# Kernel optimization log

Hardware: AMD Instinct MI355X
Metric: run time of the kernel (lower is better)

The kernel has to match this reference:

```python
import jax, jax.numpy as jnp
import numpy as np

L, H, D, A, T = 2, 8, 512, 64, 256  # layers, heads, model_dim, attention_dim, target_dim
B, S = 2, 2048
EPS = 1e-5


def _ln(x, g, b):
    m = jnp.mean(x, axis=-1, keepdims=True)
    v = jnp.mean((x - m) ** 2, axis=-1, keepdims=True)
    return (x - m) / jnp.sqrt(v + EPS) * g + b


def setup_inputs() -> dict:
    key = jax.random.key(0)
    ks = jax.random.split(key, 16)
    s = 0.02
    inp = {
        "x": jax.random.normal(ks[0], (B, S, D), jnp.float32),
        # per-head QKV projections, stacked over layers and heads
        "Wq": jax.random.normal(ks[1], (L, H, D, A), jnp.float32) * s,
        "bq": jnp.zeros((L, H, A), jnp.float32),
        "Wk": jax.random.normal(ks[2], (L, H, D, A), jnp.float32) * s,
        "bk": jnp.zeros((L, H, A), jnp.float32),
        "Wv": jax.random.normal(ks[3], (L, H, D, A), jnp.float32) * s,
        "bv": jnp.zeros((L, H, A), jnp.float32),
        # output projection of concatenated heads: [H*A, D]
        "Wo": jax.random.normal(ks[4], (L, H * A, D), jnp.float32) * s,
        "bo": jnp.zeros((L, D), jnp.float32),
        # AddNorm after attention
        "ln1_g": jnp.ones((L, D), jnp.float32),
        "ln1_b": jnp.zeros((L, D), jnp.float32),
        # FFN (hidden_dim == model_dim in this module)
        "W1": jax.random.normal(ks[5], (L, D, D), jnp.float32) * s,
        "b1": jnp.zeros((L, D), jnp.float32),
        "W2": jax.random.normal(ks[6], (L, D, D), jnp.float32) * s,
        "b2": jnp.zeros((L, D), jnp.float32),
        # AddNorm after FFN
        "ln2_g": jnp.ones((L, D), jnp.float32),
        "ln2_b": jnp.zeros((L, D), jnp.float32),
        # final projection to target_dim
        "Wp": jax.random.normal(ks[7], (D, T), jnp.float32) * s,
        "bp": jnp.zeros((T,), jnp.float32),
    }
    return inp


def reference(x, Wq, bq, Wk, bk, Wv, bv, Wo, bo, ln1_g, ln1_b,
              W1, b1, W2, b2, ln2_g, ln2_b, Wp, bp):
    scale = 1.0 / jnp.sqrt(jnp.asarray(A, x.dtype))
    for i in range(L):
        # batched per-head QKV projections (math identical to per-head Linears)
        q = jnp.einsum('bsd,hda->bhsa', x, Wq[i]) + bq[i][:, None, :]
        k = jnp.einsum('bsd,hda->bhsa', x, Wk[i]) + bk[i][:, None, :]
        v = jnp.einsum('bsd,hda->bhsa', x, Wv[i]) + bv[i][:, None, :]
        scores = jnp.einsum('bhsa,bhta->bhst', q, k) * scale  # [B,H,S,S]
        attn = jax.nn.softmax(scores, axis=-1)
        heads = jnp.einsum('bhst,bhta->bhsa', attn, v)        # [B,H,S,A]
        concat = heads.transpose(0, 2, 1, 3).reshape(x.shape[0], x.shape[1], H * A)
        mha = concat @ Wo[i] + bo[i]
        x = _ln(x + mha, ln1_g[i], ln1_b[i])
        ffn = jax.nn.relu(x @ W1[i] + b1[i]) @ W2[i] + b2[i]
        x = _ln(x + ffn, ln2_g[i], ln2_b[i])
    return x @ Wp + bp
```

## Files before the change

### kernel.cpp

```cpp
#include <hip/hip_runtime.h>
#include <hip/hip_bf16.h>

#define MDIM 4096
#define DDIM 512
#define ADIM 64
#define HHEADS 8
#define SLEN 2048
#define TDIM 256
#define SPLIT 4

typedef __attribute__((ext_vector_type(8))) short short8;
typedef __attribute__((ext_vector_type(16))) float f32x16;

__device__ __forceinline__ unsigned short f2bf(float f) {
    union { __hip_bfloat16 h; unsigned short u; } c;
    c.h = __float2bfloat16(f);
    return c.u;
}
__device__ __forceinline__ float bf2f(short s) {
    return __uint_as_float((unsigned)(unsigned short)s << 16);
}

#define N1 524288
#define N2 524288
#define NP 131072
__global__ __launch_bounds__(256) void prep_k(
    const float* __restrict__ Wq, const float* __restrict__ Wk, const float* __restrict__ Wv,
    const float* __restrict__ Wo, const float* __restrict__ W1, const float* __restrict__ W2,
    const float* __restrict__ Wp, const float* __restrict__ x,
    short* __restrict__ Wqt, short* __restrict__ Wkt, short* __restrict__ Wvt,
    short* __restrict__ Wot, short* __restrict__ W1t, short* __restrict__ W2t,
    short* __restrict__ Wpt, short* __restrict__ xbf)
{
    long idx = (long)blockIdx.x * 256 + threadIdx.x;
    if (idx < 3L * N1) {
        int t = (int)(idx / N1);
        int r = (int)(idx % N1);
        int a = r & 63, k = (r >> 6) & 511, hh = r >> 15;
        const float* src = (t == 0) ? Wq : (t == 1) ? Wk : Wv;
        short* dst = (t == 0) ? Wqt : (t == 1) ? Wkt : Wvt;
        dst[((size_t)hh << 15) + (a << 9) + k] = (short)f2bf(src[r]);
        return;
    }
    idx -= 3L * N1;
    if (idx < 3L * N2) {
        int t = (int)(idx / N2);
        int r = (int)(idx % N2);
        int n = r & 511, k = (r >> 9) & 511, i = r >> 18;
        const float* src = (t == 0) ? Wo : (t == 1) ? W1 : W2;
        short* dst = (t == 0) ? Wot : (t == 1) ? W1t : W2t;
        dst[((size_t)i << 18) + (n << 9) + k] = (short)f2bf(src[r]);
        return;
    }
    idx -= 3L * N2;
    if (idx < NP) {
        int r = (int)idx;
        int n = r & 255, k = r >> 8;
        Wpt[n * 512 + k] = (short)f2bf(Wp[r]);
        return;
    }
    idx -= NP;
    xbf[idx] = (short)f2bf(x[idx]);
}

#define LDT 66
__global__ __launch_bounds__(256, 2) void gemm_bf(
    const short* __restrict__ A, const short* __restrict__ Bt,
    const float* __restrict__ bias, void* __restrict__ Cout,
    int M, int N, int K, int flags)
{
    __shared__ short As[64 * LDT];
    __shared__ short Bs[64 * LDT];
    const int tid = threadIdx.x;
    const int wave = tid >> 6, lane = tid & 63;
    const int l31 = lane & 31, hi = lane >> 5;
    const int wm = wave >> 1, wn = wave & 1;
    const int m0 = blockIdx.y * 64, n0 = blockIdx.x * 64;

    f32x16 acc;
#pragma unroll
    for (int r = 0; r < 16; ++r) acc[r] = 0.f;

    const int sr = tid >> 2;
    const int sc = (tid & 3) * 16;

    for (int k0 = 0; k0 < K; k0 += 64) {
        __syncthreads();
        *(short8*)&As[sr * LDT + sc]     = *(const short8*)&A[(size_t)(m0 + sr) * K + k0 + sc];
        *(short8*)&As[sr * LDT + sc + 8] = *(const short8*)&A[(size_t)(m0 + sr) * K + k0 + sc + 8];
        *(short8*)&Bs[sr * LDT + sc]     = *(const short8*)&Bt[(size_t)(n0 + sr) * K + k0 + sc];
        *(short8*)&Bs[sr * LDT + sc + 8] = *(const short8*)&Bt[(size_t)(n0 + sr) * K + k0 + sc + 8];
        __syncthreads();

        short8 af[4], bfm[4];
#pragma unroll
        for (int ks = 0; ks < 4; ++ks) {
            af[ks]  = *(const short8*)&As[(wm * 32 + l31) * LDT + ks * 16 + hi * 8];
            bfm[ks] = *(const short8*)&Bs[(wn * 32 + l31) * LDT + ks * 16 + hi * 8];
        }
#pragma unroll
        for (int ks = 0; ks < 4; ++ks)
            acc = __builtin_amdgcn_mfma_f32_32x32x16_bf16(af[ks], bfm[ks], acc, 0, 0, 0);
    }

    const int col = n0 + wn * 32 + l31;
    const float bb = bias[col];
    const int rbase = m0 + wm * 32 + 4 * hi;
#pragma unroll
    for (int r = 0; r < 16; ++r) {
        int row = rbase + (r & 3) + 8 * (r >> 2);
        float v = acc[r] + bb;
        if (flags & 1) v = fmaxf(v, 0.f);
        if (flags & 2) ((short*)Cout)[(size_t)row * N + col] = (short)f2bf(v);
        else           ((float*)Cout)[(size_t)row * N + col] = v;
    }
}

#define EXPC 0.1803368801111244f

__global__ __launch_bounds__(256, 2) void qkv_bf(
    const short* __restrict__ A,
    const short* __restrict__ Wqt, const short* __restrict__ Wkt, const short* __restrict__ Wvt,
    const float* __restrict__ bq, const float* __restrict__ bk, const float* __restrict__ bv,
    short* __restrict__ Oq, short* __restrict__ Ok, short* __restrict__ Ov)
{
    __shared__ short As[128 * LDT];
    __shared__ short Bs[64 * LDT];
    const int tid = threadIdx.x;
    const int wave = tid >> 6, lane = tid & 63;
    const int l31 = lane & 31, hi = lane >> 5;
    const int wm = wave >> 1, wn = wave & 1;
    const int m0 = blockIdx.y * 128;
    const int nt = blockIdx.x;
    const int which = nt >> 3, h = nt & 7;

    const short* Bt = ((which == 0) ? Wqt : (which == 1) ? Wkt : Wvt) + (size_t)h * 64 * 512;
    const float* bias = ((which == 0) ? bq : (which == 1) ? bk : bv) + h * 64;
    short* Out = (which == 0) ? Oq : (which == 1) ? Ok : Ov;

    f32x16 acc[2];
#pragma unroll
    for (int ms = 0; ms < 2; ++ms)
#pragma unroll
        for (int r = 0; r < 16; ++r) acc[ms][r] = 0.f;

    const int sr = tid >> 3;
    const int sc = (tid & 7) * 8;

    for (int k0 = 0; k0 < 512; k0 += 64) {
        __syncthreads();
#pragma unroll
        for (int p = 0; p < 4; ++p)
            *(short8*)&As[(p * 32 + sr) * LDT + sc] =
                *(const short8*)&A[(size_t)(m0 + p * 32 + sr) * 512 + k0 + sc];
#pragma unroll
        for (int p = 0; p < 2; ++p)
            *(short8*)&Bs[(p * 32 + sr) * LDT + sc] =
                *(const short8*)&Bt[(size_t)(p * 32 + sr) * 512 + k0 + sc];
        __syncthreads();

        short8 af[2][4], bfm[4];
#pragma unroll
        for (int ms = 0; ms < 2; ++ms)
#pragma unroll
            for (int ks = 0; ks < 4; ++ks)
                af[ms][ks] = *(const short8*)&As[(wm * 64 + ms * 32 + l31) * LDT + ks * 16 + hi * 8];
#pragma unroll
        for (int ks = 0; ks < 4; ++ks)
            bfm[ks] = *(const short8*)&Bs[(wn * 32 + l31) * LDT + ks * 16 + hi * 8];
#pragma unroll
        for (int ms = 0; ms < 2; ++ms)
#pragma unroll
            for (int ks = 0; ks < 4; ++ks)
                acc[ms] = __builtin_amdgcn_mfma_f32_32x32x16_bf16(af[ms][ks], bfm[ks], acc[ms], 0, 0, 0);
    }

    const int a = wn * 32 + l31;
    const float bb = bias[a];
    const int b = m0 >> 11;
    const int sb = (m0 & (SLEN - 1)) + wm * 64;
    const int bh = b * HHEADS + h;

    if (which == 0) {
        short* Ob = Out + (size_t)bh * SLEN * 64;
#pragma unroll
        for (int ms = 0; ms < 2; ++ms)
#pragma unroll
            for (int r = 0; r < 16; ++r) {
                int s = sb + ms * 32 + (r & 3) + 8 * (r >> 2) + 4 * hi;
                Ob[(size_t)s * 64 + a] = (short)f2bf((acc[ms][r] + bb) * EXPC);
            }
    } else if (which == 1) {
        short* Ob = Out + (size_t)bh * SLEN * 64;
#pragma unroll
        for (int ms = 0; ms < 2; ++ms)
#pragma unroll
            for (int r = 0; r < 16; ++r) {
                int s = sb + ms * 32 + (r & 3) + 8 * (r >> 2) + 4 * hi;
                Ob[(size_t)s * 64 + a] = (short)f2bf(acc[ms][r] + bb);
            }
    } else {
        short* Ob = Out + ((size_t)bh * 64 + a) * SLEN;
#pragma unroll
        for (int ms = 0; ms < 2; ++ms)
#pragma unroll
            for (int g = 0; g < 4; ++g) {
                int s = sb + ms * 32 + 8 * g + 4 * hi;
                ushort4 w;
                w.x = f2bf(acc[ms][4 * g + 0] + bb);
                w.y = f2bf(acc[ms][4 * g + 1] + bb);
                w.z = f2bf(acc[ms][4 * g + 2] + bb);
                w.w = f2bf(acc[ms][4 * g + 3] + bb);
                *(ushort4*)&Ob[s] = w;
            }
    }
}

__global__ __launch_bounds__(256, 2) void attn_mfma(
    const short* __restrict__ Qb, const short* __restrict__ Kb,
    const short* __restrict__ Vtb, short* __restrict__ Op,
    float* __restrict__ lp)
{
    __shared__ short Ks[64 * 72];
    __shared__ short Vs[64 * 72];

    const int tid = threadIdx.x;
    const int wid = tid >> 6;
    const int lane = tid & 63;
    const int l31 = lane & 31;
    const int hi = lane >> 5;

    const int qt = blockIdx.x;
    const int bh = blockIdx.y;
    const int sp = blockIdx.z;

    const short* Qg = Qb + (size_t)bh * SLEN * 64;
    const short* Kg = Kb + (size_t)bh * SLEN * 64;
    const short* Vg = Vtb + (size_t)bh * 64 * SLEN;

    const int q0 = qt * 256 + wid * 64;

    short8 qf[2][4];
#pragma unroll
    for (int nt = 0; nt < 2; ++nt)
#pragma unroll
        for (int ks = 0; ks < 4; ++ks)
            qf[nt][ks] = *(const short8*)&Qg[(size_t)(q0 + nt * 32 + l31) * 64 + ks * 16 + hi * 8];

    f32x16 oacc[2][2];
    float lsum[2] = {0.f, 0.f};
#pragma unroll
    for (int nt = 0; nt < 2; ++nt)
#pragma unroll
        for (int dt = 0; dt < 2; ++dt)
#pragma unroll
            for (int r = 0; r < 16; ++r) oacc[nt][dt][r] = 0.f;

    const int srow = tid >> 2;
    const int sch = (tid & 3) * 16;
    const int kbase = sp * (SLEN / SPLIT);

    short8 rk0 = *(const short8*)&Kg[(size_t)(kbase + srow) * 64 + sch];
    short8 rk1 = *(const short8*)&Kg[(size_t)(kbase + srow) * 64 + sch + 8];
    short8 rv0 = *(const short8*)&Vg[(size_t)srow * SLEN + kbase + sch];
    short8 rv1 = *(const short8*)&Vg[(size_t)srow * SLEN + kbase + sch + 8];

    for (int kt = 0; kt < 8; ++kt) {
        __syncthreads();
        *(short8*)&Ks[srow * 72 + sch]     = rk0;
        *(short8*)&Ks[srow * 72 + sch + 8] = rk1;
        *(short8*)&Vs[srow * 72 + sch]     = rv0;
        *(short8*)&Vs[srow * 72 + sch + 8] = rv1;
        __syncthreads();

        if (kt < 7) {
            const int k0n = kbase + (kt + 1) * 64;
            rk0 = *(const short8*)&Kg[(size_t)(k0n + srow) * 64 + sch];
            rk1 = *(const short8*)&Kg[(size_t)(k0n + srow) * 64 + sch + 8];
            rv0 = *(const short8*)&Vg[(size_t)srow * SLEN + k0n + sch];
            rv1 = *(const short8*)&Vg[(size_t)srow * SLEN + k0n + sch + 8];
        }

        short8 kf[2][4], vf[2][4];
#pragma unroll
        for (int mt = 0; mt < 2; ++mt)
#pragma unroll
            for (int ks = 0; ks < 4; ++ks)
                kf[mt][ks] = *(const short8*)&Ks[(mt * 32 + l31) * 72 + ks * 16 + hi * 8];
#pragma unroll
        for (int dt = 0; dt < 2; ++dt)
#pragma unroll
            for (int p = 0; p < 4; ++p)
                vf[dt][p] = *(const short8*)&Vs[(dt * 32 + l31) * 72 + p * 16 + hi * 8];

#pragma unroll
        for (int nt = 0; nt < 2; ++nt) {
            f32x16 sacc[2];
            __builtin_amdgcn_s_setprio(1);
#pragma unroll
            for (int mt = 0; mt < 2; ++mt) {
                f32x16 s;
#pragma unroll
                for (int r = 0; r < 16; ++r) s[r] = 0.f;
#pragma unroll
                for (int ks = 0; ks < 4; ++ks)
                    s = __builtin_amdgcn_mfma_f32_32x32x16_bf16(kf[mt][ks], qf[nt][ks], s, 0, 0, 0);
                sacc[mt] = s;
            }
            __builtin_amdgcn_s_setprio(0);

            int2 pk[2][4];
#pragma unroll
            for (int mt = 0; mt < 2; ++mt)
#pragma unroll
                for (int g = 0; g < 4; ++g) {
                    unsigned a0 = __float_as_uint(__builtin_amdgcn_exp2f(sacc[mt][4 * g + 0]));
                    unsigned a1 = __float_as_uint(__builtin_amdgcn_exp2f(sacc[mt][4 * g + 1]));
                    unsigned a2 = __float_as_uint(__builtin_amdgcn_exp2f(sacc[mt][4 * g + 2]));
                    unsigned a3 = __float_as_uint(__builtin_amdgcn_exp2f(sacc[mt][4 * g + 3]));
                    float t0 = __uint_as_float(a0 & 0xffff0000u);
                    float t1 = __uint_as_float(a1 & 0xffff0000u);
                    float t2 = __uint_as_float(a2 & 0xffff0000u);
                    float t3 = __uint_as_float(a3 & 0xffff0000u);
                    lsum[nt] += (t0 + t1) + (t2 + t3);
                    pk[mt][g].x = (int)__builtin_amdgcn_perm(a1, a0, 0x07060302u);
                    pk[mt][g].y = (int)__builtin_amdgcn_perm(a3, a2, 0x07060302u);
                }

            int2 xch[2][2];
#pragma unroll
            for (int mt = 0; mt < 2; ++mt)
#pragma unroll
                for (int h2 = 0; h2 < 2; ++h2) {
                    int2 v = hi ? pk[mt][2 * h2] : pk[mt][2 * h2 + 1];
                    xch[mt][h2].x = __shfl_xor(v.x, 32);
                    xch[mt][h2].y = __shfl_xor(v.y, 32);
                }

            __builtin_amdgcn_s_setprio(1);
#pragma unroll
            for (int p = 0; p < 4; ++p) {
                const int mt = p >> 1, h2 = p & 1;
                const int ga = 2 * h2, gb = 2 * h2 + 1;
                const int2 X = xch[mt][h2];
                union { int4 i; short8 s; } u;
                u.i.x = hi ? X.x : pk[mt][ga].x;
                u.i.y = hi ? X.y : pk[mt][ga].y;
                u.i.z = hi ? pk[mt][gb].x : X.x;
                u.i.w = hi ? pk[mt][gb].y : X.y;
#pragma unroll
                for (int dt = 0; dt < 2; ++dt)
                    oacc[nt][dt] = __builtin_amdgcn_mfma_f32_32x32x16_bf16(u.s, vf[dt][p], oacc[nt][dt], 0, 0, 0);
            }
            __builtin_amdgcn_s_setprio(0);
        }
    }

#pragma unroll
    for (int nt = 0; nt < 2; ++nt) {
        float lt = lsum[nt] + __shfl_xor(lsum[nt], 32);
        if (hi == 0)
            lp[((size_t)(sp * 16 + bh)) * SLEN + q0 + nt * 32 + l31] = lt;
#pragma unroll
        for (int dt = 0; dt < 2; ++dt) {
#pragma unroll
            for (int r = 0; r < 16; ++r) {
                int qrow = (r & 3) + 8 * (r >> 2) + 4 * hi;
                size_t addr = (((size_t)(sp * 16 + bh)) * SLEN + (q0 + nt * 32 + qrow)) * 64 + dt * 32 + l31;
                Op[addr] = (short)f2bf(oacc[nt][dt][r]);
            }
        }
    }
}

__global__ __launch_bounds__(256) void merge_k(
    const short* __restrict__ Op, const float* __restrict__ lp,
    short* __restrict__ hc)
{
    const int g = blockIdx.x * 256 + threadIdx.x;
    const int d4 = g & 15;
    const int s = (g >> 4) & (SLEN - 1);
    const int bh = g >> 15;

    float o[4] = {0.f, 0.f, 0.f, 0.f};
    float ls = 0.f;
#pragma unroll
    for (int sp = 0; sp < SPLIT; ++sp) {
        const size_t base = (((size_t)(sp * 16 + bh)) * SLEN + s);
        ushort4 u4 = *(const ushort4*)&Op[base * 64 + d4 * 4];
        o[0] += bf2f((short)u4.x); o[1] += bf2f((short)u4.y);
        o[2] += bf2f((short)u4.z); o[3] += bf2f((short)u4.w);
        ls += lp[base];
    }
    const int b = bh >> 3, h = bh & 7;
    const float inv = 1.f / ls;
    ushort4 w;
    w.x = f2bf(o[0] * inv); w.y = f2bf(o[1] * inv);
    w.z = f2bf(o[2] * inv); w.w = f2bf(o[3] * inv);
    *(ushort4*)&hc[((size_t)(b * SLEN + s)) * DDIM + h * 64 + d4 * 4] = w;
}

__global__ __launch_bounds__(256) void addnorm_bf(
    short* __restrict__ X, const float* __restrict__ Y,
    const float* __restrict__ g, const float* __restrict__ beta)
{
    const int lane = threadIdx.x & 63;
    const int t = blockIdx.x * 4 + (threadIdx.x >> 6);
    short* xr = X + (size_t)t * DDIM;
    const float* yr = Y + (size_t)t * DDIM;
    const int c0 = lane * 8;

    short8 x8 = *(const short8*)&xr[c0];
    float4 y0 = *(const float4*)&yr[c0];
    float4 y1 = *(const float4*)&yr[c0 + 4];
    float v[8];
    v[0] = bf2f(x8[0]) + y0.x; v[1] = bf2f(x8[1]) + y0.y;
    v[2] = bf2f(x8[2]) + y0.z; v[3] = bf2f(x8[3]) + y0.w;
    v[4] = bf2f(x8[4]) + y1.x; v[5] = bf2f(x8[5]) + y1.y;
    v[6] = bf2f(x8[6]) + y1.z; v[7] = bf2f(x8[7]) + y1.w;

    float s1 = 0.f, s2 = 0.f;
#pragma unroll
    for (int j = 0; j < 8; ++j) { s1 += v[j]; s2 += v[j] * v[j]; }
#pragma unroll
    for (int off = 1; off < 64; off <<= 1) {
        s1 += __shfl_xor(s1, off);
        s2 += __shfl_xor(s2, off);
    }
    float mean = s1 * (1.0f / DDIM);
    float var = s2 * (1.0f / DDIM) - mean * mean;
    float rstd = rsqrtf(var + 1e-5f);

    float4 ga = *(const float4*)&g[c0];
    float4 gb = *(const float4*)&g[c0 + 4];
    float4 ba = *(const float4*)&beta[c0];
    float4 bb = *(const float4*)&beta[c0 + 4];
    float gg[8] = {ga.x, ga.y, ga.z, ga.w, gb.x, gb.y, gb.z, gb.w};
    float bt[8] = {ba.x, ba.y, ba.z, ba.w, bb.x, bb.y, bb.z, bb.w};

    short8 o8;
#pragma unroll
    for (int j = 0; j < 8; ++j)
        o8[j] = (short)f2bf((v[j] - mean) * rstd * gg[j] + bt[j]);
    *(short8*)&xr[c0] = o8;
}

extern "C" void kernel_launch(void* const* d_in, const int* in_sizes, int n_in,
                              void* d_out, int out_size, void* d_ws, size_t ws_size,
                              hipStream_t stream)
{
    (void)in_sizes; (void)n_in; (void)out_size; (void)ws_size;
    const float* x   = (const float*)d_in[0];
    const float* Wq  = (const float*)d_in[1];
    const float* bq  = (const float*)d_in[2];
    const float* Wk  = (const float*)d_in[3];
    const float* bk  = (const float*)d_in[4];
    const float* Wv  = (const float*)d_in[5];
    const float* bv  = (const float*)d_in[6];
    const float* Wo  = (const float*)d_in[7];
    const float* bo  = (const float*)d_in[8];
    const float* g1  = (const float*)d_in[9];
    const float* be1 = (const float*)d_in[10];
    const float* W1  = (const float*)d_in[11];
    const float* b1  = (const float*)d_in[12];
    const float* W2  = (const float*)d_in[13];
    const float* b2  = (const float*)d_in[14];
    const float* g2  = (const float*)d_in[15];
    const float* be2 = (const float*)d_in[16];
    const float* Wp  = (const float*)d_in[17];
    const float* bp  = (const float*)d_in[18];

    char* wsb = (char*)d_ws;
    const size_t MB = 1024 * 1024;
    short* xbf   = (short*)(wsb + 0);
    short* Qbuf  = (short*)(wsb + 4 * MB);
    short* Kbuf  = (short*)(wsb + 8 * MB);
    short* Vtbuf = (short*)(wsb + 12 * MB);
    short* Opart = (short*)(wsb + 16 * MB);
    float* y     = (float*)(wsb + 16 * MB);
    short* hidbf = (short*)(wsb + 24 * MB);
    float* lpart = (float*)(wsb + 32 * MB);
    short* hcbf  = Qbuf;
    short* Wqt   = (short*)(wsb + 33 * MB);
    short* Wkt   = (short*)(wsb + 34 * MB);
    short* Wvt   = (short*)(wsb + 35 * MB);
    short* Wot   = (short*)(wsb + 36 * MB);
    short* W1t   = (short*)(wsb + 37 * MB);
    short* W2t   = (short*)(wsb + 38 * MB);
    short* Wpt   = (short*)(wsb + 39 * MB);

    prep_k<<<20992, 256, 0, stream>>>(Wq, Wk, Wv, Wo, W1, W2, Wp, x,
                                      Wqt, Wkt, Wvt, Wot, W1t, W2t, Wpt, xbf);

    for (int i = 0; i < 2; ++i) {
        const size_t wOffQ = (size_t)i * 262144;
        const size_t wOffS = (size_t)i * 262144;
        qkv_bf<<<dim3(24, 32), 256, 0, stream>>>(
            xbf, Wqt + wOffQ, Wkt + wOffQ, Wvt + wOffQ,
            bq + i * 512, bk + i * 512, bv + i * 512,
            Qbuf, Kbuf, Vtbuf);
        attn_mfma<<<dim3(8, 16, SPLIT), 256, 0, stream>>>(Qbuf, Kbuf, Vtbuf, Opart, lpart);
        merge_k<<<2048, 256, 0, stream>>>(Opart, lpart, hcbf);
        gemm_bf<<<dim3(8, 64), 256, 0, stream>>>(
            hcbf, Wot + wOffS, bo + i * 512, y, MDIM, DDIM, DDIM, 0);
        addnorm_bf<<<1024, 256, 0, stream>>>(xbf, y, g1 + i * 512, be1 + i * 512);
        gemm_bf<<<dim3(8, 64), 256, 0, stream>>>(
            xbf, W1t + wOffS, b1 + i * 512, hidbf, MDIM, DDIM, DDIM, 3);
        gemm_bf<<<dim3(8, 64), 256, 0, stream>>>(
            hidbf, W2t + wOffS, b2 + i * 512, y, MDIM, DDIM, DDIM, 0);
        addnorm_bf<<<1024, 256, 0, stream>>>(xbf, y, g2 + i * 512, be2 + i * 512);
    }
    gemm_bf<<<dim3(4, 64), 256, 0, stream>>>(
        xbf, Wpt, bp, (float*)d_out, MDIM, TDIM, DDIM, 0);
}
```

Baseline: 297.5 us.

## Fuse split-K attention merge into attention kernel via intra-block wave reduction

Restructures attention so each block handles 64 queries and its four waves each cover a quarter of the key range, reducing partial outputs through shared memory instead of writing bf16 partials and running a separate merge kernel. K/V fragments are now loaded directly from global memory per wave rather than staged through LDS with double-buffered prefetch. A swizzled 1D grid is used to group blocks by head. This removes one launch and the partial-output round trip through global memory, but drops K/V sharing across waves and adds a large fp32 LDS buffer that may reduce occupancy.

```diff
diff --git a/kernel.cpp b/kernel.cpp
--- a/kernel.cpp
+++ b/kernel.cpp
@@ -7,7 +7,6 @@
 #define HHEADS 8
 #define SLEN 2048
 #define TDIM 256
-#define SPLIT 4
 
 typedef __attribute__((ext_vector_type(8))) short short8;
 typedef __attribute__((ext_vector_type(16))) float f32x16;
@@ -218,11 +217,10 @@
 
 __global__ __launch_bounds__(256, 2) void attn_mfma(
     const short* __restrict__ Qb, const short* __restrict__ Kb,
-    const short* __restrict__ Vtb, short* __restrict__ Op,
-    float* __restrict__ lp)
-{
-    __shared__ short Ks[64 * 72];
-    __shared__ short Vs[64 * 72];
+    const short* __restrict__ Vtb, short* __restrict__ hc)
+{
+    __shared__ float Ols[4][64][66];
+    __shared__ float Lls[4][64];
 
     const int tid = threadIdx.x;
     const int wid = tid >> 6;
@@ -230,15 +228,16 @@
     const int l31 = lane & 31;
     const int hi = lane >> 5;
 
-    const int qt = blockIdx.x;
-    const int bh = blockIdx.y;
-    const int sp = blockIdx.z;
+    const int wg = blockIdx.x;
+    const int swz = (wg & 7) * 64 + (wg >> 3);
+    const int qt = swz & 31;
+    const int bh = swz >> 5;
 
     const short* Qg = Qb + (size_t)bh * SLEN * 64;
     const short* Kg = Kb + (size_t)bh * SLEN * 64;
     const short* Vg = Vtb + (size_t)bh * 64 * SLEN;
 
-    const int q0 = qt * 256 + wid * 64;
+    const int q0 = qt * 64;
 
     short8 qf[2][4];
 #pragma unroll
@@ -256,42 +255,23 @@
 #pragma unroll
             for (int r = 0; r < 16; ++r) oacc[nt][dt][r] = 0.f;
 
-    const int srow = tid >> 2;
-    const int sch = (tid & 3) * 16;
-    const int kbase = sp * (SLEN / SPLIT);
-
-    short8 rk0 = *(const short8*)&Kg[(size_t)(kbase + srow) * 64 + sch];
-    short8 rk1 = *(const short8*)&Kg[(size_t)(kbase + srow) * 64 + sch + 8];
-    short8 rv0 = *(const short8*)&Vg[(size_t)srow * SLEN + kbase + sch];
-    short8 rv1 = *(const short8*)&Vg[(size_t)srow * SLEN + kbase + sch + 8];
-
+    const int kw = wid * (SLEN / 4);
+
+#pragma unroll 1
     for (int kt = 0; kt < 8; ++kt) {
-        __syncthreads();
-        *(short8*)&Ks[srow * 72 + sch]     = rk0;
-        *(short8*)&Ks[srow * 72 + sch + 8] = rk1;
-        *(short8*)&Vs[srow * 72 + sch]     = rv0;
-        *(short8*)&Vs[srow * 72 + sch + 8] = rv1;
-        __syncthreads();
-
-        if (kt < 7) {
-            const int k0n = kbase + (kt + 1) * 64;
-            rk0 = *(const short8*)&Kg[(size_t)(k0n + srow) * 64 + sch];
-            rk1 = *(const short8*)&Kg[(size_t)(k0n + srow) * 64 + sch + 8];
-            rv0 = *(const short8*)&Vg[(size_t)srow * SLEN + k0n + sch];
-            rv1 = *(const short8*)&Vg[(size_t)srow * SLEN + k0n + sch + 8];
-        }
+        const int k0 = kw + kt * 64;
 
         short8 kf[2][4], vf[2][4];
 #pragma unroll
         for (int mt = 0; mt < 2; ++mt)
 #pragma unroll
             for (int ks = 0; ks < 4; ++ks)
-                kf[mt][ks] = *(const short8*)&Ks[(mt * 32 + l31) * 72 + ks * 16 + hi * 8];
+                kf[mt][ks] = *(const short8*)&Kg[(size_t)(k0 + mt * 32 + l31) * 64 + ks * 16 + hi * 8];
 #pragma unroll
         for (int dt = 0; dt < 2; ++dt)
 #pragma unroll
             for (int p = 0; p < 4; ++p)
-                vf[dt][p] = *(const short8*)&Vs[(dt * 32 + l31) * 72 + p * 16 + hi * 8];
+                vf[dt][p] = *(const short8*)&Vg[(size_t)(dt * 32 + l31) * SLEN + k0 + p * 16 + hi * 8];
 
 #pragma unroll
         for (int nt = 0; nt < 2; ++nt) {
@@ -359,45 +339,32 @@
 #pragma unroll
     for (int nt = 0; nt < 2; ++nt) {
         float lt = lsum[nt] + __shfl_xor(lsum[nt], 32);
-        if (hi == 0)
-            lp[((size_t)(sp * 16 + bh)) * SLEN + q0 + nt * 32 + l31] = lt;
-#pragma unroll
-        for (int dt = 0; dt < 2; ++dt) {
+        if (hi == 0) Lls[wid][nt * 32 + l31] = lt;
+#pragma unroll
+        for (int dt = 0; dt < 2; ++dt)
 #pragma unroll
             for (int r = 0; r < 16; ++r) {
-                int qrow = (r & 3) + 8 * (r >> 2) + 4 * hi;
-                size_t addr = (((size_t)(sp * 16 + bh)) * SLEN + (q0 + nt * 32 + qrow)) * 64 + dt * 32 + l31;
-                Op[addr] = (short)f2bf(oacc[nt][dt][r]);
-            }
+                int q = nt * 32 + (r & 3) + 8 * (r >> 2) + 4 * hi;
+                Ols[wid][q][dt * 32 + l31] = oacc[nt][dt][r];
+            }
+    }
+    __syncthreads();
+
+    const int b = bh >> 3, h = bh & 7;
+    const int q = tid >> 2;
+    const int c0 = (tid & 3) * 16;
+    const float inv = 1.f / (Lls[0][q] + Lls[1][q] + Lls[2][q] + Lls[3][q]);
+    short* orow = hc + ((size_t)(b * SLEN + q0 + q)) * DDIM + h * 64 + c0;
+#pragma unroll
+    for (int half = 0; half < 2; ++half) {
+        short8 o8;
+#pragma unroll
+        for (int j = 0; j < 8; ++j) {
+            int d = c0 + half * 8 + j;
+            o8[j] = (short)f2bf((Ols[0][q][d] + Ols[1][q][d] + Ols[2][q][d] + Ols[3][q][d]) * inv);
         }
-    }
-}
-
-__global__ __launch_bounds__(256) void merge_k(
-    const short* __restrict__ Op, const float* __restrict__ lp,
-    short* __restrict__ hc)
-{
-    const int g = blockIdx.x * 256 + threadIdx.x;
-    const int d4 = g & 15;
-    const int s = (g >> 4) & (SLEN - 1);
-    const int bh = g >> 15;
-
-    float o[4] = {0.f, 0.f, 0.f, 0.f};
-    float ls = 0.f;
-#pragma unroll
-    for (int sp = 0; sp < SPLIT; ++sp) {
-        const size_t base = (((size_t)(sp * 16 + bh)) * SLEN + s);
-        ushort4 u4 = *(const ushort4*)&Op[base * 64 + d4 * 4];
-        o[0] += bf2f((short)u4.x); o[1] += bf2f((short)u4.y);
-        o[2] += bf2f((short)u4.z); o[3] += bf2f((short)u4.w);
-        ls += lp[base];
-    }
-    const int b = bh >> 3, h = bh & 7;
-    const float inv = 1.f / ls;
-    ushort4 w;
-    w.x = f2bf(o[0] * inv); w.y = f2bf(o[1] * inv);
-    w.z = f2bf(o[2] * inv); w.w = f2bf(o[3] * inv);
-    *(ushort4*)&hc[((size_t)(b * SLEN + s)) * DDIM + h * 64 + d4 * 4] = w;
+        *(short8*)&orow[half * 8] = o8;
+    }
 }
 
 __global__ __launch_bounds__(256) void addnorm_bf(
@@ -476,11 +443,9 @@
     short* Qbuf  = (short*)(wsb + 4 * MB);
     short* Kbuf  = (short*)(wsb + 8 * MB);
     short* Vtbuf = (short*)(wsb + 12 * MB);
-    short* Opart = (short*)(wsb + 16 * MB);
-    float* y     = (float*)(wsb + 16 * MB);
-    short* hidbf = (short*)(wsb + 24 * MB);
-    float* lpart = (float*)(wsb + 32 * MB);
-    short* hcbf  = Qbuf;
+    short* hcbf  = (short*)(wsb + 16 * MB);
+    float* y     = (float*)(wsb + 20 * MB);
+    short* hidbf = (short*)(wsb + 28 * MB);
     short* Wqt   = (short*)(wsb + 33 * MB);
     short* Wkt   = (short*)(wsb + 34 * MB);
     short* Wvt   = (short*)(wsb + 35 * MB);
@@ -499,8 +464,7 @@
             xbf, Wqt + wOffQ, Wkt + wOffQ, Wvt + wOffQ,
             bq + i * 512, bk + i * 512, bv + i * 512,
             Qbuf, Kbuf, Vtbuf);
-        attn_mfma<<<dim3(8, 16, SPLIT), 256, 0, stream>>>(Qbuf, Kbuf, Vtbuf, Opart, lpart);
-        merge_k<<<2048, 256, 0, stream>>>(Opart, lpart, hcbf);
+        attn_mfma<<<512, 256, 0, stream>>>(Qbuf, Kbuf, Vtbuf, hcbf);
         gemm_bf<<<dim3(8, 64), 256, 0, stream>>>(
             hcbf, Wot + wOffS, bo + i * 512, y, MDIM, DDIM, DDIM, 0);
         addnorm_bf<<<1024, 256, 0, stream>>>(xbf, y, g1 + i * 512, be1 + i * 512);
```

After: 304.2 us. +2.2%, slower.
